# Kernel optimization log

Hardware: AMD Instinct MI355X
Metric: run time of the kernel (lower is better)

Reference implementation:

```python
import jax, jax.numpy as jnp
from jax import lax
import numpy as np

EPSILON = 22.6  # Cech radius; ~mean pairwise distance of N(0,1) points in 256-d


def _betti1(x, eps):
    """Faithful port of compute_betti_number for one epsilon. x: (B,T,C)."""
    B, T, C = x.shape
    # pairwise squared distances; compare d2 < eps^2 == (dist < eps), avoids sqrt
    sq = jnp.sum(x * x, axis=-1)                                  # (B,T)
    d2 = sq[:, :, None] + sq[:, None, :] - 2.0 * jnp.einsum('btc,bsc->bts', x, x)
    adj = d2 < (eps * eps)                                        # (B,T,T) bool; diagonal True (dist 0 < eps), matching torch
    adj = lax.stop_gradient(adj)                                  # original detaches x before topology
    # original: n_edges = np.sum(adjacency) // 2, diagonal included
    n_edges = jnp.sum(adj, axis=(1, 2)).astype(jnp.int32) // 2    # (B,)
    # connected components via min-label propagation + pointer jumping
    labels0 = jnp.broadcast_to(jnp.arange(T, dtype=jnp.int32), (B, T))

    def cond(state):
        return state[1]

    def body(state):
        labels, _ = state
        # min label among neighbors (diag True includes self)
        prop = jnp.min(jnp.where(adj, labels[:, None, :], T), axis=2).astype(jnp.int32)
        new = jnp.minimum(labels, prop)
        new = jnp.take_along_axis(new, new, axis=1)               # pointer jump -> O(log) convergence
        return new, jnp.any(new != labels)

    labels, _ = lax.while_loop(cond, body, (labels0, jnp.array(True)))
    # converged label = min index in component -> count roots
    n_comp = jnp.sum(labels == jnp.arange(T, dtype=jnp.int32)[None, :], axis=1).astype(jnp.int32)
    betti1 = jnp.maximum(0, n_edges - T + n_comp)                 # max(0, E - V + C)
    return betti1


def reference(x_before, x_after):
    betti_before = _betti1(x_before, EPSILON)
    betti_after = _betti1(x_after, EPSILON)
    diff = betti_after.astype(jnp.float32) - betti_before.astype(jnp.float32)
    return jnp.mean(diff * diff)


def setup_inputs() -> dict:
    key = jax.random.key(0)
    k1, k2 = jax.random.split(key)
    B, T, C = 4, 4096, 256
    x_before = jax.random.normal(k1, (B, T, C), dtype=jnp.float32)
    x_after = jax.random.normal(k2, (B, T, C), dtype=jnp.float32)
    return {"x_before": x_before, "x_after": x_after}
```

## Files before the change

kernel.cpp:

```cpp
#include <hip/hip_runtime.h>
#include <stdint.h>

#define TDIM 4096
#define CDIM 256
#define NMAT 8
#define NPAIR 272

typedef __attribute__((ext_vector_type(8))) __bf16 bf16x8;
typedef __attribute__((ext_vector_type(4))) float f32x4;

__device__ __forceinline__ unsigned short f2bf(float f) {
  unsigned int u = __float_as_uint(f);
  return (unsigned short)((u + 0x7FFFu + ((u >> 16) & 1u)) >> 16);
}
__device__ __forceinline__ void g2lds16(const void* g, void* l) {
  __builtin_amdgcn_global_load_lds((__attribute__((address_space(1))) void*)(void*)g,
                                   (__attribute__((address_space(3))) void*)l, 16, 0, 0);
}
__device__ __forceinline__ unsigned long long shfl_xor_u64(unsigned long long v, int m) {
  int lo = __shfl_xor((int)(unsigned int)(v & 0xFFFFFFFFull), m);
  int hi = __shfl_xor((int)(unsigned int)(v >> 32), m);
  return ((unsigned long long)(unsigned int)hi << 32) | (unsigned int)lo;
}

__global__ __launch_bounds__(256) void prep_kernel(
    const float* __restrict__ xb, const float* __restrict__ xa,
    unsigned short* __restrict__ xhi, float* __restrict__ sq) {
  const int wid = threadIdx.x >> 6, lane = threadIdx.x & 63;
  const int gr = blockIdx.x * 4 + wid;
  const int mb = gr >> 12;
  const size_t rowoff = (size_t)gr * CDIM;
  const float* src = (mb < 4) ? (xb + rowoff) : (xa + rowoff - (size_t)4 * TDIM * CDIM);

  float4 v = ((const float4*)src)[lane];
  float vv[4] = {v.x, v.y, v.z, v.w};
  unsigned short h[4];
  float ss = 0.f;
#pragma unroll
  for (int c = 0; c < 4; ++c) {
    h[c] = f2bf(vv[c]);
    ss += vv[c] * vv[c];
  }
  *(ushort4*)&xhi[rowoff + lane * 4] = make_ushort4(h[0], h[1], h[2], h[3]);
#pragma unroll
  for (int off = 32; off; off >>= 1) ss += __shfl_down(ss, off);
  if (lane == 0) sq[gr] = ss;
}

__global__ __launch_bounds__(256) void prep4_kernel(
    const float* __restrict__ src0, unsigned short* __restrict__ xhi,
    float* __restrict__ sq4) {
  const int wid = threadIdx.x >> 6, lane = threadIdx.x & 63;
  const int gr = blockIdx.x * 4 + wid;
  const size_t rowoff = (size_t)gr * CDIM;
  float4 v = ((const float4*)(src0 + rowoff))[lane];
  float vv[4] = {v.x, v.y, v.z, v.w};
  unsigned short h[4];
  float ss = 0.f;
#pragma unroll
  for (int c = 0; c < 4; ++c) {
    h[c] = f2bf(vv[c]);
    ss += vv[c] * vv[c];
  }
  *(ushort4*)&xhi[rowoff + lane * 4] = make_ushort4(h[0], h[1], h[2], h[3]);
#pragma unroll
  for (int off = 32; off; off >>= 1) ss += __shfl_down(ss, off);
  if (lane == 0) sq4[gr] = ss;
}

__global__ __launch_bounds__(512, 4) void gram_kernel(
    const unsigned short* __restrict__ xhi, const float* __restrict__ sq,
    unsigned long long* __restrict__ adj, unsigned int* __restrict__ edgepart,
    int ep_base, int mb_base, int mbits) {
  __shared__ unsigned short lds[3 * 128 * 64];
  __shared__ unsigned int wcnt[8];

  const int tid = threadIdx.x;
  const int wid = tid >> 6, lane = tid & 63;
  const int wr = wid >> 2;
  const int wcq = wid & 3;
  const int t = wcq >> 1, wc = wcq & 1;

  const int mbl = blockIdx.x & ((1 << mbits) - 1);
  const int mb = mb_base + mbl;
  int rem = blockIdx.x >> mbits;
  int ti = 0;
  while (rem >= ((33 - ti) >> 1)) { rem -= (33 - ti) >> 1; ++ti; }
  const int tj0 = ti + 2 * rem;
  const int hasT1 = (tj0 < 31);
  const int tj1 = hasT1 ? tj0 + 1 : tj0;

  const unsigned short* hi = xhi + (size_t)mbl * TDIM * CDIM;
  const float* sqm = sq + (size_t)mb * TDIM;

  f32x4 acc[4][4] = {};

  const int ldrow = (lane >> 3);
  const int ldcol = ((lane & 7) ^ ldrow) * 8;

  for (int ks = 0; ks < 4; ++ks) {
    const int kcol = ks * 64;
    __syncthreads();
#pragma unroll
    for (int i = 0; i < 6; ++i) {
      const int c = wid * 6 + i;
      const int tile = c >> 4, cit = c & 15;
      const int trow = (tile == 0) ? ti : ((tile == 1) ? tj0 : tj1);
      const int row = cit * 8 + ldrow;
      g2lds16(hi + (size_t)(trow * 128 + row) * CDIM + kcol + ldcol,
              &lds[tile * 8192 + cit * 512]);
    }
    asm volatile("s_waitcnt vmcnt(0)" ::: "memory");
    __syncthreads();
#pragma unroll
    for (int kk = 0; kk < 2; ++kk) {
      bf16x8 a[4], b[4];
      const int hi16 = lane >> 4;
#pragma unroll
      for (int m = 0; m < 4; ++m) {
        const int row = wr * 64 + m * 16 + (lane & 15);
        a[m] = *(const bf16x8*)&lds[row * 64 + (((kk * 4 + hi16) ^ (row & 7)) * 8)];
      }
#pragma unroll
      for (int n = 0; n < 4; ++n) {
        const int row = wc * 64 + n * 16 + (lane & 15);
        b[n] = *(const bf16x8*)&lds[(1 + t) * 8192 + row * 64 +
                                    (((kk * 4 + hi16) ^ (row & 7)) * 8)];
      }
#pragma unroll
      for (int m = 0; m < 4; ++m)
#pragma unroll
        for (int n = 0; n < 4; ++n)
          acc[m][n] = __builtin_amdgcn_mfma_f32_16x16x32_bf16(a[m], b[n], acc[m][n], 0, 0, 0);
    }
  }

  const float EPS2 = (float)(22.6 * 22.6);
  unsigned long long* adjm = adj + (size_t)mb * TDIM * 64;
  const int gt = (lane >> 2) & 3;
  const int mtgt = lane >> 4, rtgt = lane & 3;
  const int tjt = t ? tj1 : tj0;
  const int active = (t == 0) || hasT1;

  unsigned int myc = 0;
  if (active) {
    float4 srv[4];
#pragma unroll
    for (int m = 0; m < 4; ++m)
      srv[m] = *(const float4*)&sqm[ti * 128 + wr * 64 + m * 16 + (lane >> 4) * 4];
    float scv[4];
#pragma unroll
    for (int n = 0; n < 4; ++n) scv[n] = sqm[tjt * 128 + wc * 64 + n * 16 + (lane & 15)];

    unsigned long long vrow = 0;
#pragma unroll
    for (int m = 0; m < 4; ++m) {
#pragma unroll
      for (int r = 0; r < 4; ++r) {
        const float srr = ((const float*)&srv[m])[r];
        unsigned long long bl[4];
#pragma unroll
        for (int n = 0; n < 4; ++n) {
          const float d2 = srr + scv[n] - 2.0f * acc[m][n][r];
          bl[n] = __ballot(d2 < EPS2);
        }
        if (m == mtgt && r == rtgt)
          vrow = ((bl[0] >> (16 * gt)) & 0xFFFFULL)         | (((bl[1] >> (16 * gt)) & 0xFFFFULL) << 16) |
                 (((bl[2] >> (16 * gt)) & 0xFFFFULL) << 32) | (((bl[3] >> (16 * gt)) & 0xFFFFULL) << 48);
      }
    }
    adjm[(size_t)(ti * 128 + wr * 64 + lane) * 64 + tjt * 2 + wc] = vrow;

    {
      unsigned int pc = (unsigned int)__popcll(vrow);
#pragma unroll
      for (int off = 32; off; off >>= 1) pc += __shfl_down(pc, off);
      myc = (ti != tjt) ? pc * 2u : pc;
    }

    if (ti != tjt) {
      const unsigned long long mk[6] = {
          0x5555555555555555ull, 0x3333333333333333ull, 0x0F0F0F0F0F0F0F0Full,
          0x00FF00FF00FF00FFull, 0x0000FFFF0000FFFFull, 0x00000000FFFFFFFFull};
#pragma unroll
      for (int s = 0; s < 6; ++s) {
        const int d = 1 << s;
        const unsigned long long mkk = mk[s];
        unsigned long long tt = shfl_xor_u64(vrow, d);
        if ((lane & d) == 0) vrow = (vrow & mkk) | ((tt & mkk) << d);
        else                 vrow = (vrow & ~mkk) | ((tt & ~mkk) >> d);
      }
      adjm[(size_t)(tjt * 128 + wc * 64 + lane) * 64 + ti * 2 + wr] = vrow;
    }
  }
  if (lane == 0) wcnt[wid] = myc;

  __syncthreads();
  if (tid == 0)
    edgepart[ep_base + blockIdx.x] = wcnt[0] + wcnt[1] + wcnt[2] + wcnt[3] +
                                     wcnt[4] + wcnt[5] + wcnt[6] + wcnt[7];
}

__global__ __launch_bounds__(1024) void cc_iter_kernel(const unsigned long long* __restrict__ adj,
                                                       int* __restrict__ ncomp) {
  __shared__ int lab[TDIM];
  __shared__ int nxt[TDIM];
  __shared__ int changed;
  __shared__ int croots;
  const int mb = blockIdx.x;
  const unsigned long long* A = adj + (size_t)mb * TDIM * 64;
  const int tid = threadIdx.x;

  for (int i = tid; i < TDIM; i += 1024) {
    unsigned long long w0 = A[(size_t)i * 64];
    nxt[i] = w0 ? (__ffsll(w0) - 1) : i;
  }
  __syncthreads();
  for (int i = tid; i < TDIM; i += 1024) lab[i] = nxt[nxt[i]];
  __syncthreads();

  for (int it = 0; it < 96; ++it) {
    if (tid == 0) changed = 0;
    __syncthreads();
    for (int i = tid; i < TDIM; i += 1024) {
      const int cur = lab[i];
      int mn = cur;
      if (cur > 0) {
        for (int wd = 0; wd < 64 && mn > 0; ++wd) {
          unsigned long long w = A[(size_t)i * 64 + wd];
          while (w && mn > 0) {
            const int bit = __ffsll(w) - 1;
            w &= w - 1;
            mn = min(mn, lab[wd * 64 + bit]);
          }
        }
        if (mn < cur) changed = 1;
      }
      nxt[i] = mn;
    }
    __syncthreads();
    const int ch = changed;
    for (int i = tid; i < TDIM; i += 1024) lab[i] = nxt[nxt[i]];
    __syncthreads();
    if (!ch) break;
  }

  if (tid == 0) croots = 0;
  __syncthreads();
  int c = 0;
  for (int i = tid; i < TDIM; i += 1024) c += (lab[i] == i);
  atomicAdd(&croots, c);
  __syncthreads();
  if (tid == 0) ncomp[mb] = croots;
}

__global__ __launch_bounds__(512) void final_kernel(const unsigned int* __restrict__ edgepart,
                                                    const int* __restrict__ ncomp,
                                                    float* __restrict__ out, int big) {
  __shared__ unsigned long long es[8];
  const int wid = threadIdx.x >> 6, lane = threadIdx.x & 63;
  unsigned long long s = 0;
  if (big) {
    for (int k = lane; k < NPAIR; k += 64) s += edgepart[k * 8 + wid];
  } else {
    const int base = (wid < 4) ? 0 : 4 * NPAIR;
    const int m4 = wid & 3;
    for (int k = lane; k < NPAIR; k += 64) s += edgepart[base + k * 4 + m4];
  }
#pragma unroll
  for (int off = 32; off; off >>= 1) s += __shfl_down(s, off);
  if (lane == 0) es[wid] = s;
  __syncthreads();
  if (threadIdx.x == 0) {
    double acc = 0.0;
    for (int b = 0; b < 4; ++b) {
      long long e0 = (long long)(es[b] >> 1);
      long long bet0 = e0 - TDIM + (long long)ncomp[b];
      if (bet0 < 0) bet0 = 0;
      long long e1 = (long long)(es[4 + b] >> 1);
      long long bet1 = e1 - TDIM + (long long)ncomp[4 + b];
      if (bet1 < 0) bet1 = 0;
      double d = (double)(bet1 - bet0);
      acc += d * d;
    }
    out[0] = (float)(acc * 0.25);
  }
}

extern "C" void kernel_launch(void* const* d_in, const int* in_sizes, int n_in,
                              void* d_out, int out_size, void* d_ws, size_t ws_size,
                              hipStream_t stream) {
  (void)in_sizes; (void)n_in; (void)out_size;
  const float* xb = (const float*)d_in[0];
  const float* xa = (const float*)d_in[1];
  char* ws = (char*)d_ws;

  const bool big = (ws_size == 0) || (ws_size >= ((size_t)34 << 20));

  if (big) {
    const size_t XHI_OFF = 0;
    const size_t ADJ_OFF = (size_t)NMAT * TDIM * CDIM * 2;
    const size_t SQ_OFF  = ADJ_OFF + (size_t)NMAT * TDIM * 64 * 8;
    const size_t NC_OFF  = SQ_OFF + (size_t)NMAT * TDIM * 4;
    const size_t EDGE_OFF = NC_OFF + 64;

    unsigned short* xhi = (unsigned short*)(ws + XHI_OFF);
    unsigned long long* adj = (unsigned long long*)(ws + ADJ_OFF);
    float* sq = (float*)(ws + SQ_OFF);
    int* ncomp = (int*)(ws + NC_OFF);
    unsigned int* edgepart = (unsigned int*)(ws + EDGE_OFF);

    prep_kernel<<<NMAT * TDIM / 4, 256, 0, stream>>>(xb, xa, xhi, sq);
    gram_kernel<<<NMAT * NPAIR, 512, 0, stream>>>(xhi, sq, adj, edgepart, 0, 0, 3);
    cc_iter_kernel<<<NMAT, 1024, 0, stream>>>(adj, ncomp);
    final_kernel<<<1, 512, 0, stream>>>(edgepart, ncomp, (float*)d_out, 1);
  } else {
    const size_t XHI_OFF = 0;
    const size_t ADJ_OFF = (size_t)4 * TDIM * CDIM * 2;
    const size_t SQ_OFF  = ADJ_OFF + (size_t)NMAT * TDIM * 64 * 8;
    const size_t NC_OFF  = SQ_OFF + (size_t)NMAT * TDIM * 4;
    const size_t EDGE_OFF = NC_OFF + 64;

    unsigned short* xhi = (unsigned short*)(ws + XHI_OFF);
    unsigned long long* adj = (unsigned long long*)(ws + ADJ_OFF);
    float* sq = (float*)(ws + SQ_OFF);
    int* ncomp = (int*)(ws + NC_OFF);
    unsigned int* edgepart = (unsigned int*)(ws + EDGE_OFF);

    prep4_kernel<<<TDIM, 256, 0, stream>>>(xb, xhi, sq);
    gram_kernel<<<4 * NPAIR, 512, 0, stream>>>(xhi, sq, adj, edgepart, 0, 0, 2);
    prep4_kernel<<<TDIM, 256, 0, stream>>>(xa, xhi, sq + (size_t)4 * TDIM);
    gram_kernel<<<4 * NPAIR, 512, 0, stream>>>(xhi, sq, adj, edgepart, 4 * NPAIR, 4, 2);
    cc_iter_kernel<<<NMAT, 1024, 0, stream>>>(adj, ncomp);
    final_kernel<<<1, 512, 0, stream>>>(edgepart, ncomp, (float*)d_out, 0);
  }
}
```

Before: 79.38 us.

## Share each row tile across three column tiles per gram block

Each gram block now stages one row tile plus three column tiles, up from two, and runs 12 waves (768 threads), so the row tile in LDS is reused across more output tiles. The upper-triangular pair enumeration changes from groups of two to groups of three, which cuts the block count from 272 to 187 per matrix and lowers redundant row-tile loads. The cost is more LDS per block (64 KB), a larger block that may reduce occupancy, and more idle waves in the clamped tail tiles near the diagonal.

```diff
diff --git a/kernel.cpp b/kernel.cpp
--- a/kernel.cpp
+++ b/kernel.cpp
@@ -4,7 +4,7 @@
 #define TDIM 4096
 #define CDIM 256
 #define NMAT 8
-#define NPAIR 272
+#define NPAIR3 187
 
 typedef __attribute__((ext_vector_type(8))) __bf16 bf16x8;
 typedef __attribute__((ext_vector_type(4))) float f32x4;
@@ -68,27 +68,27 @@
   if (lane == 0) sq4[gr] = ss;
 }
 
-__global__ __launch_bounds__(512, 4) void gram_kernel(
+__global__ __launch_bounds__(768, 4) void gram_kernel(
     const unsigned short* __restrict__ xhi, const float* __restrict__ sq,
     unsigned long long* __restrict__ adj, unsigned int* __restrict__ edgepart,
     int ep_base, int mb_base, int mbits) {
-  __shared__ unsigned short lds[3 * 128 * 64];
-  __shared__ unsigned int wcnt[8];
+  __shared__ unsigned short lds[4 * 128 * 64];
+  __shared__ unsigned int wcnt[12];
 
   const int tid = threadIdx.x;
   const int wid = tid >> 6, lane = tid & 63;
-  const int wr = wid >> 2;
-  const int wcq = wid & 3;
-  const int t = wcq >> 1, wc = wcq & 1;
+  const int wr = wid / 6;
+  const int wq = wid % 6;
+  const int t = wq >> 1, wc = wq & 1;
 
   const int mbl = blockIdx.x & ((1 << mbits) - 1);
   const int mb = mb_base + mbl;
   int rem = blockIdx.x >> mbits;
   int ti = 0;
-  while (rem >= ((33 - ti) >> 1)) { rem -= (33 - ti) >> 1; ++ti; }
-  const int tj0 = ti + 2 * rem;
-  const int hasT1 = (tj0 < 31);
-  const int tj1 = hasT1 ? tj0 + 1 : tj0;
+  while (rem >= (34 - ti) / 3) { rem -= (34 - ti) / 3; ++ti; }
+  const int tj0 = ti + 3 * rem;
+  const int tjc1 = (tj0 + 1 <= 31) ? tj0 + 1 : 31;
+  const int tjc2 = (tj0 + 2 <= 31) ? tj0 + 2 : 31;
 
   const unsigned short* hi = xhi + (size_t)mbl * TDIM * CDIM;
   const float* sqm = sq + (size_t)mb * TDIM;
@@ -101,11 +101,10 @@
   for (int ks = 0; ks < 4; ++ks) {
     const int kcol = ks * 64;
     __syncthreads();
-#pragma unroll
-    for (int i = 0; i < 6; ++i) {
-      const int c = wid * 6 + i;
+    for (int c = wid; c < 64; c += 12) {
       const int tile = c >> 4, cit = c & 15;
-      const int trow = (tile == 0) ? ti : ((tile == 1) ? tj0 : tj1);
+      const int trow = (tile == 0) ? ti :
+                       ((tile == 1) ? tj0 : ((tile == 2) ? tjc1 : tjc2));
       const int row = cit * 8 + ldrow;
       g2lds16(hi + (size_t)(trow * 128 + row) * CDIM + kcol + ldcol,
               &lds[tile * 8192 + cit * 512]);
@@ -139,8 +138,9 @@
   unsigned long long* adjm = adj + (size_t)mb * TDIM * 64;
   const int gt = (lane >> 2) & 3;
   const int mtgt = lane >> 4, rtgt = lane & 3;
-  const int tjt = t ? tj1 : tj0;
-  const int active = (t == 0) || hasT1;
+  const int tjt_raw = tj0 + t;
+  const int active = (tjt_raw <= 31);
+  const int tjt = active ? tjt_raw : 31;
 
   unsigned int myc = 0;
   if (active) {
@@ -196,9 +196,12 @@
   if (lane == 0) wcnt[wid] = myc;
 
   __syncthreads();
-  if (tid == 0)
-    edgepart[ep_base + blockIdx.x] = wcnt[0] + wcnt[1] + wcnt[2] + wcnt[3] +
-                                     wcnt[4] + wcnt[5] + wcnt[6] + wcnt[7];
+  if (tid == 0) {
+    unsigned int s = 0;
+#pragma unroll
+    for (int w = 0; w < 12; ++w) s += wcnt[w];
+    edgepart[ep_base + blockIdx.x] = s;
+  }
 }
 
 __global__ __launch_bounds__(1024) void cc_iter_kernel(const unsigned long long* __restrict__ adj,
@@ -261,11 +264,11 @@
   const int wid = threadIdx.x >> 6, lane = threadIdx.x & 63;
   unsigned long long s = 0;
   if (big) {
-    for (int k = lane; k < NPAIR; k += 64) s += edgepart[k * 8 + wid];
+    for (int k = lane; k < NPAIR3; k += 64) s += edgepart[k * 8 + wid];
   } else {
-    const int base = (wid < 4) ? 0 : 4 * NPAIR;
+    const int base = (wid < 4) ? 0 : 4 * NPAIR3;
     const int m4 = wid & 3;
-    for (int k = lane; k < NPAIR; k += 64) s += edgepart[base + k * 4 + m4];
+    for (int k = lane; k < NPAIR3; k += 64) s += edgepart[base + k * 4 + m4];
   }
 #pragma unroll
   for (int off = 32; off; off >>= 1) s += __shfl_down(s, off);
@@ -311,7 +314,7 @@
     unsigned int* edgepart = (unsigned int*)(ws + EDGE_OFF);
 
     prep_kernel<<<NMAT * TDIM / 4, 256, 0, stream>>>(xb, xa, xhi, sq);
-    gram_kernel<<<NMAT * NPAIR, 512, 0, stream>>>(xhi, sq, adj, edgepart, 0, 0, 3);
+    gram_kernel<<<NMAT * NPAIR3, 768, 0, stream>>>(xhi, sq, adj, edgepart, 0, 0, 3);
     cc_iter_kernel<<<NMAT, 1024, 0, stream>>>(adj, ncomp);
     final_kernel<<<1, 512, 0, stream>>>(edgepart, ncomp, (float*)d_out, 1);
   } else {
@@ -328,9 +331,9 @@
     unsigned int* edgepart = (unsigned int*)(ws + EDGE_OFF);
 
     prep4_kernel<<<TDIM, 256, 0, stream>>>(xb, xhi, sq);
-    gram_kernel<<<4 * NPAIR, 512, 0, stream>>>(xhi, sq, adj, edgepart, 0, 0, 2);
+    gram_kernel<<<4 * NPAIR3, 768, 0, stream>>>(xhi, sq, adj, edgepart, 0, 0, 2);
     prep4_kernel<<<TDIM, 256, 0, stream>>>(xa, xhi, sq + (size_t)4 * TDIM);
-    gram_kernel<<<4 * NPAIR, 512, 0, stream>>>(xhi, sq, adj, edgepart, 4 * NPAIR, 4, 2);
+    gram_kernel<<<4 * NPAIR3, 768, 0, stream>>>(xhi, sq, adj, edgepart, 4 * NPAIR3, 4, 2);
     cc_iter_kernel<<<NMAT, 1024, 0, stream>>>(adj, ncomp);
     final_kernel<<<1, 512, 0, stream>>>(edgepart, ncomp, (float*)d_out, 0);
   }
```

Measured after the change: 94.65 us. 1.19x slower.
